# Kernel optimization log

Hardware: AMD Instinct MI355X
Metric: run time of the kernel (lower is better)

## Reference

```python
import jax, jax.numpy as jnp
import numpy as np

D = 1024
H = 16
HD = D // H
FF = 4 * D
EPS = 1e-5


def _layernorm(x, scale, shift):
    # Faithful to the torch module: unbiased std (ddof=1), eps added to std.
    mean = jnp.mean(x, axis=-1, keepdims=True)
    var = jnp.sum((x - mean) ** 2, axis=-1, keepdims=True) / (x.shape[-1] - 1)
    std = jnp.sqrt(var)
    return shift + scale * (x - mean) / (std + EPS)


def _gelu(x):
    c = jnp.sqrt(jnp.asarray(2.0 / jnp.pi, dtype=x.dtype))
    return 0.5 * x * (1.0 + jnp.tanh(c * (x + 0.044715 * x ** 3)))


def setup_inputs() -> dict:
    key = jax.random.key(0)
    ks = jax.random.split(key, 8)
    B, S = 2, 2048
    inv = 1.0 / np.sqrt(D)
    x = jax.random.normal(ks[0], (B, S, D), dtype=jnp.float32)
    scale1 = jnp.ones((D,), jnp.float32)
    shift1 = jnp.zeros((D,), jnp.float32)
    Wqkv = jax.random.normal(ks[1], (3 * D, D), jnp.float32) * inv  # torch layout [out,in]
    Wo_w = jax.random.normal(ks[2], (D, D), jnp.float32) * inv
    Wo_b = jnp.zeros((D,), jnp.float32)
    scale2 = jnp.ones((D,), jnp.float32)
    shift2 = jnp.zeros((D,), jnp.float32)
    W1 = jax.random.normal(ks[3], (FF, D), jnp.float32) * inv
    b1 = jnp.zeros((FF,), jnp.float32)
    W2 = jax.random.normal(ks[4], (D, FF), jnp.float32) * (1.0 / np.sqrt(FF))
    b2 = jnp.zeros((D,), jnp.float32)
    return {"x": x, "scale1": scale1, "shift1": shift1, "Wqkv": Wqkv,
            "Wo_w": Wo_w, "Wo_b": Wo_b, "scale2": scale2, "shift2": shift2,
            "W1": W1, "b1": b1, "W2": W2, "b2": b2}


def reference(x, scale1, shift1, Wqkv, Wo_w, Wo_b, scale2, shift2, W1, b1, W2, b2):
    B, S, _ = x.shape
    # --- pre-norm attention ---
    h = _layernorm(x, scale1, shift1)
    qkv = jnp.einsum('bsd,ed->bse', h, Wqkv)  # [B,S,3D]
    q, k, v = jnp.split(qkv, 3, axis=-1)
    q = q.reshape(B, S, H, HD).transpose(0, 2, 1, 3)  # [B,H,S,HD]
    k = k.reshape(B, S, H, HD).transpose(0, 2, 1, 3)
    v = v.reshape(B, S, H, HD).transpose(0, 2, 1, 3)
    scores = jnp.einsum('bhqd,bhkd->bhqk', q, k) / jnp.sqrt(jnp.asarray(HD, x.dtype))
    causal = jnp.triu(jnp.ones((S, S), dtype=bool), k=1)
    scores = jnp.where(causal, -jnp.inf, scores)
    weights = jax.nn.softmax(scores, axis=-1)
    attn = jnp.einsum('bhqk,bhkd->bhqd', weights, v)
    attn = attn.transpose(0, 2, 1, 3).reshape(B, S, D)
    attn = jnp.einsum('bsd,ed->bse', attn, Wo_w) + Wo_b
    x = x + attn
    # --- pre-norm MLP ---
    h2 = _layernorm(x, scale2, shift2)
    m = _gelu(jnp.einsum('bsd,fd->bsf', h2, W1) + b1)
    m = jnp.einsum('bsf,df->bsd', m, W2) + b2
    return x + m
```

## Files before the change

### kernel.cpp

```cpp
#include <hip/hip_runtime.h>
#include <cstdint>
#include <cstddef>

typedef __bf16 bf16;
typedef __bf16 v8bf __attribute__((ext_vector_type(8)));
typedef __bf16 v4bf __attribute__((ext_vector_type(4)));
typedef float  v4f  __attribute__((ext_vector_type(4)));

#define D_MODEL 1024
#define FF_DIM  4096
#define SEQ     2048
#define NTOK    4096
#define NH      16
#define HDIM    64

#define GLOAD_LDS16(g, l) \
    __builtin_amdgcn_global_load_lds((const __attribute__((address_space(1))) void*)(g), \
                                     (__attribute__((address_space(3))) void*)(l), 16, 0, 0)

#define QSCALE 0.18033688011112042f
#define SHIFT2 -28.853900817779268f

#define BARRIER()    asm volatile("s_barrier" ::: "memory")
#define WAIT_VM8()   asm volatile("s_waitcnt vmcnt(8)" ::: "memory")
#define WAIT_VM0()   asm volatile("s_waitcnt vmcnt(0)" ::: "memory")
#define WAIT_LGKM0() asm volatile("s_waitcnt lgkmcnt(0)" ::: "memory")

__global__ __launch_bounds__(256) void prep_kernel(
    const float* __restrict__ Wqkv, const float* __restrict__ Wo,
    const float* __restrict__ W1, const float* __restrict__ W2,
    bf16* __restrict__ Wqkv_b, bf16* __restrict__ Wo_b,
    bf16* __restrict__ W1_b, bf16* __restrict__ W2_b) {
    int u = blockIdx.x * 256 + threadIdx.x;
    const float* src; bf16* dst; int idx;
    if (u < 786432)       { src = Wqkv; dst = Wqkv_b; idx = u * 4; }
    else if (u < 1048576) { src = Wo;   dst = Wo_b;   idx = (u - 786432) * 4; }
    else if (u < 2097152) { src = W1;   dst = W1_b;   idx = (u - 1048576) * 4; }
    else                  { src = W2;   dst = W2_b;   idx = (u - 2097152) * 4; }
    float4 v = *(const float4*)(src + idx);
    dst[idx + 0] = (bf16)v.x;
    dst[idx + 1] = (bf16)v.y;
    dst[idx + 2] = (bf16)v.z;
    dst[idx + 3] = (bf16)v.w;
}

__global__ __launch_bounds__(256) void layernorm_kernel(
    const float* __restrict__ x, const float* __restrict__ scale,
    const float* __restrict__ shift, bf16* __restrict__ out) {
    int row = blockIdx.x;
    int t = threadIdx.x;
    const float* xr = x + (size_t)row * D_MODEL;
    float4 v = *(const float4*)(xr + t * 4);
    float s  = v.x + v.y + v.z + v.w;
    float sq = v.x * v.x + v.y * v.y + v.z * v.z + v.w * v.w;
    #pragma unroll
    for (int o = 1; o < 64; o <<= 1) {
        s  += __shfl_xor(s, o);
        sq += __shfl_xor(sq, o);
    }
    __shared__ float ws[8];
    int wv = t >> 6;
    if ((t & 63) == 0) { ws[wv * 2] = s; ws[wv * 2 + 1] = sq; }
    __syncthreads();
    s  = ws[0] + ws[2] + ws[4] + ws[6];
    sq = ws[1] + ws[3] + ws[5] + ws[7];
    float mean = s * (1.0f / D_MODEL);
    float var  = (sq - (float)D_MODEL * mean * mean) * (1.0f / (D_MODEL - 1));
    var = fmaxf(var, 0.0f);
    float inv = 1.0f / (sqrtf(var) + 1e-5f);
    #pragma unroll
    for (int j = 0; j < 4; ++j) {
        int c = t * 4 + j;
        float xv = (&v.x)[j];
        out[(size_t)row * D_MODEL + c] = (bf16)(shift[c] + scale[c] * (xv - mean) * inv);
    }
}

__global__ __launch_bounds__(256) void transpose_v(
    const bf16* __restrict__ vb, bf16* __restrict__ vt) {
    int bh = blockIdx.x >> 5;
    int ts = blockIdx.x & 31;
    int t = threadIdx.x;
    __shared__ bf16 T[64][72];
    const bf16* src = vb + ((size_t)bh * SEQ + ts * 64) * HDIM;
    #pragma unroll
    for (int half = 0; half < 2; ++half) {
        int s = (t >> 3) + half * 32;
        int d0 = (t & 7) * 8;
        v8bf vv = *(const v8bf*)(src + (size_t)s * HDIM + d0);
        #pragma unroll
        for (int j = 0; j < 8; ++j) T[d0 + j][s] = vv[j];
    }
    __syncthreads();
    bf16* dst = vt + (size_t)bh * HDIM * SEQ + ts * 64;
    int d = t >> 2;
    #pragma unroll
    for (int cc = 0; cc < 2; ++cc) {
        int c = (t & 3) + cc * 4;
        v8bf o = *(const v8bf*)(&T[d][c * 8]);
        *(v8bf*)(dst + (size_t)d * SEQ + c * 8) = o;
    }
}

template <int EPI>
__global__ __launch_bounds__(256) void gemm_nt(
    const bf16* __restrict__ A, const bf16* __restrict__ Bw,
    const float* __restrict__ bias, const float* __restrict__ resid,
    float* __restrict__ outf, bf16* __restrict__ ob0,
    bf16* __restrict__ ob1, bf16* __restrict__ ob2,
    int M, int N, int K, int klen) {
    __shared__ __align__(16) bf16 As[128 * 64];
    __shared__ __align__(16) bf16 Bs[128 * 64];
    int gx = gridDim.x;
    int lin = blockIdx.y * gx + blockIdx.x;
    int grpsz = 16 * gx;
    int group = lin / grpsz;
    int rem = lin - group * grpsz;
    int m_t = group * 16 + (rem & 15);
    int n_t = rem >> 4;
    int m0 = m_t * 128, n0 = n_t * 128;
    int kstart = blockIdx.z * klen;
    int t = threadIdx.x;
    int lane = t & 63, wave = t >> 6;
    int wm = wave >> 1, wn = wave & 1;
    int quad = lane >> 4, l16 = lane & 15;

    int srow8 = lane >> 3;
    int schunk = (lane & 7) ^ srow8;
    const bf16* agp = A  + (size_t)(m0 + wave * 8 + srow8) * K + kstart + schunk * 8;
    const bf16* bgp = Bw + (size_t)(n0 + wave * 8 + srow8) * K + kstart + schunk * 8;
    size_t row32 = (size_t)32 * K;

    v4f acc[4][4];
    #pragma unroll
    for (int i = 0; i < 4; ++i)
        #pragma unroll
        for (int j = 0; j < 4; ++j)
            acc[i][j] = (v4f){0.f, 0.f, 0.f, 0.f};

    int rsw = l16 & 7;
    for (int kk = 0; kk < klen; kk += 64) {
        __syncthreads();
        #pragma unroll
        for (int ii = 0; ii < 4; ++ii) {
            GLOAD_LDS16(agp + ii * row32 + kk, &As[ii * 2048 + wave * 512]);
            GLOAD_LDS16(bgp + ii * row32 + kk, &Bs[ii * 2048 + wave * 512]);
        }
        __syncthreads();
        #pragma unroll
        for (int h = 0; h < 2; ++h) {
            v8bf af[4], bfr[4];
            #pragma unroll
            for (int i = 0; i < 4; ++i)
                af[i] = *(const v8bf*)(&As[(wm * 64 + i * 16 + l16) * 64 + (((h * 4 + quad) ^ rsw)) * 8]);
            #pragma unroll
            for (int j = 0; j < 4; ++j)
                bfr[j] = *(const v8bf*)(&Bs[(wn * 64 + j * 16 + l16) * 64 + (((h * 4 + quad) ^ rsw)) * 8]);
            #pragma unroll
            for (int i = 0; i < 4; ++i)
                #pragma unroll
                for (int j = 0; j < 4; ++j)
                    acc[i][j] = __builtin_amdgcn_mfma_f32_16x16x32_bf16(af[i], bfr[j], acc[i][j], 0, 0, 0);
        }
    }

    #pragma unroll
    for (int i = 0; i < 4; ++i) {
        #pragma unroll
        for (int j = 0; j < 4; ++j) {
            #pragma unroll
            for (int r = 0; r < 4; ++r) {
                float v = acc[i][j][r];
                int row = m0 + wm * 64 + i * 16 + quad * 4 + r;
                int col = n0 + wn * 64 + j * 16 + l16;
                if (EPI == 1) {
                    size_t o = (size_t)row * N + col;
                    outf[o] = resid[o] + v + bias[col];
                }
            }
        }
    }
}

template <int EPI>
__global__ __launch_bounds__(512, 2) void gemm2_nt(
    const bf16* __restrict__ A, const bf16* __restrict__ Bw,
    const float* __restrict__ bias, bf16* __restrict__ ob0,
    bf16* __restrict__ ob1, bf16* __restrict__ ob2,
    int M, int N, int K, int klen) {
    __shared__ __align__(16) bf16 smA[2][256 * 64];
    __shared__ __align__(16) bf16 smB[2][256 * 64];

    int gx = gridDim.x, gy = gridDim.y;
    int nwg = gx * gy;
    int lin = blockIdx.y * gx + blockIdx.x;
    int q8 = nwg >> 3;
    int swz = (lin & 7) * q8 + (lin >> 3);
    int m_t = swz % gy;
    int n_t = swz / gy;
    int m0 = m_t * 256, n0 = n_t * 256;
    int kstart = blockIdx.z * klen;
    int t = threadIdx.x;
    int lane = t & 63, wave = t >> 6;
    int wm = wave >> 2, wn = wave & 3;
    int quad = lane >> 4, l16 = lane & 15;

    int srow8 = lane >> 3;
    int schunk = (lane & 7) ^ srow8;
    const bf16* aA = A  + (size_t)(m0 + wave * 8 + srow8) * K + kstart + schunk * 8;
    const bf16* bB = Bw + (size_t)(n0 + wave * 8 + srow8) * K + kstart + schunk * 8;
    size_t row64 = (size_t)64 * K;
    int NT = klen >> 6;

    v4f acc[8][4];
    #pragma unroll
    for (int i = 0; i < 8; ++i)
        #pragma unroll
        for (int j = 0; j < 4; ++j)
            acc[i][j] = (v4f){0.f, 0.f, 0.f, 0.f};

    auto stage = [&](int c, int kt) {
        size_t ko = (size_t)kt * 64;
        const bf16* ag = aA + ko;
        const bf16* bg = bB + ko;
        #pragma unroll
        for (int q = 0; q < 4; ++q) {
            GLOAD_LDS16(ag + q * row64, &smA[c][q * 4096 + wave * 512]);
            GLOAD_LDS16(bg + q * row64, &smB[c][q * 4096 + wave * 512]);
        }
    };

    stage(0, 0);
    if (NT > 1) { stage(1, 1); WAIT_VM8(); } else { WAIT_VM0(); }
    BARRIER();

    int rx = l16 & 7;
    int ch0 = (quad ^ rx) * 8;
    int ch1 = ch0 ^ 32;
    int arow = (wm * 128 + l16) * 64;
    int brow = (wn * 64 + l16) * 64;

    for (int kt = 0; kt < NT; ++kt) {
        int c = kt & 1;
        const bf16* Ab = &smA[c][arow];
        const bf16* Bb = &smB[c][brow];
        v8bf a[4][2], b[4][2];
        #pragma unroll
        for (int i = 0; i < 4; ++i) {
            a[i][0] = *(const v8bf*)(Ab + i * 1024 + ch0);
            a[i][1] = *(const v8bf*)(Ab + i * 1024 + ch1);
        }
        #pragma unroll
        for (int j = 0; j < 4; ++j) {
            b[j][0] = *(const v8bf*)(Bb + j * 1024 + ch0);
            b[j][1] = *(const v8bf*)(Bb + j * 1024 + ch1);
        }
        __builtin_amdgcn_s_setprio(1);
        #pragma unroll
        for (int i = 0; i < 4; ++i)
            #pragma unroll
            for (int j = 0; j < 2; ++j) {
                acc[i][j] = __builtin_amdgcn_mfma_f32_16x16x32_bf16(a[i][0], b[j][0], acc[i][j], 0, 0, 0);
                acc[i][j] = __builtin_amdgcn_mfma_f32_16x16x32_bf16(a[i][1], b[j][1], acc[i][j], 0, 0, 0);
            }
        __builtin_amdgcn_s_setprio(0);
        __builtin_amdgcn_s_setprio(1);
        #pragma unroll
        for (int i = 0; i < 4; ++i)
            #pragma unroll
            for (int j = 2; j < 4; ++j) {
                acc[i][j] = __builtin_amdgcn_mfma_f32_16x16x32_bf16(a[i][0], b[j][0], acc[i][j], 0, 0, 0);
                acc[i][j] = __builtin_amdgcn_mfma_f32_16x16x32_bf16(a[i][1], b[j][1], acc[i][j], 0, 0, 0);
            }
        __builtin_amdgcn_s_setprio(0);
        #pragma unroll
        for (int i = 0; i < 4; ++i) {
            a[i][0] = *(const v8bf*)(Ab + 4096 + i * 1024 + ch0);
            a[i][1] = *(const v8bf*)(Ab + 4096 + i * 1024 + ch1);
        }
        __builtin_amdgcn_s_setprio(1);
        #pragma unroll
        for (int i = 0; i < 4; ++i)
            #pragma unroll
            for (int j = 0; j < 2; ++j) {
                acc[i + 4][j] = __builtin_amdgcn_mfma_f32_16x16x32_bf16(a[i][0], b[j][0], acc[i + 4][j], 0, 0, 0);
                acc[i + 4][j] = __builtin_amdgcn_mfma_f32_16x16x32_bf16(a[i][1], b[j][1], acc[i + 4][j], 0, 0, 0);
            }
        __builtin_amdgcn_s_setprio(0);
        WAIT_LGKM0();
        BARRIER();
        if (kt + 2 < NT) stage(c, kt + 2);
        __builtin_amdgcn_s_setprio(1);
        #pragma unroll
        for (int i = 0; i < 4; ++i)
            #pragma unroll
            for (int j = 2; j < 4; ++j) {
                acc[i + 4][j] = __builtin_amdgcn_mfma_f32_16x16x32_bf16(a[i][0], b[j][0], acc[i + 4][j], 0, 0, 0);
                acc[i + 4][j] = __builtin_amdgcn_mfma_f32_16x16x32_bf16(a[i][1], b[j][1], acc[i + 4][j], 0, 0, 0);
            }
        __builtin_amdgcn_s_setprio(0);
        if (kt + 1 < NT) {
            if (kt + 2 < NT) WAIT_VM8();
            else             WAIT_VM0();
            BARRIER();
        }
    }

    #pragma unroll
    for (int i = 0; i < 8; ++i) {
        #pragma unroll
        for (int j = 0; j < 4; ++j) {
            #pragma unroll
            for (int r = 0; r < 4; ++r) {
                float v = acc[i][j][r];
                int row = m0 + wm * 128 + i * 16 + quad * 4 + r;
                int col = n0 + wn * 64 + j * 16 + l16;
                if (EPI == 0) {
                    int which = col >> 10, rr = col & 1023;
                    int h = rr >> 6, d = rr & 63;
                    int bb = row >> 11, sI = row & 2047;
                    size_t dst = (((size_t)(bb * NH + h)) * SEQ + sI) * HDIM + d;
                    if (which == 0)      ob0[dst] = (bf16)(v * QSCALE);
                    else if (which == 1) ob1[dst] = (bf16)v;
                    else                 ob2[dst] = (bf16)v;
                } else if (EPI == 2) {
                    float u = v + bias[col];
                    float y = 1.5957691216057308f * (u + 0.044715f * u * u * u);
                    float g = u * __builtin_amdgcn_rcpf(1.0f + __expf(-y));
                    ob0[(size_t)row * N + col] = (bf16)g;
                } else {
                    ob0[(size_t)blockIdx.z * M * N + (size_t)row * N + col] = (bf16)v;
                }
            }
        }
    }
}

__global__ __launch_bounds__(256) void combine_w2(
    const bf16* __restrict__ part, const float* __restrict__ x1,
    const float* __restrict__ b2, float* __restrict__ out) {
    int i = (blockIdx.x * 256 + threadIdx.x) * 4;
    int col = i & (D_MODEL - 1);
    float4 xv = *(const float4*)(x1 + i);
    float4 bv = *(const float4*)(b2 + col);
    float4 r;
    r.x = xv.x + bv.x; r.y = xv.y + bv.y; r.z = xv.z + bv.z; r.w = xv.w + bv.w;
    #pragma unroll
    for (int z = 0; z < 4; ++z) {
        v4bf p = *(const v4bf*)(part + (size_t)z * NTOK * D_MODEL + i);
        r.x += (float)p[0]; r.y += (float)p[1]; r.z += (float)p[2]; r.w += (float)p[3];
    }
    *(float4*)(out + i) = r;
}

__device__ __forceinline__ void attn_process_tile(
    int kv, int qwb, int quad, int l16,
    const bf16* Ks, const bf16* Vs, bf16* Pw, const v8bf& ones,
    const v8bf& qf0, const v8bf& qf1, v4f (&o)[4], v4f& o5) {
    #pragma unroll
    for (int hh = 0; hh < 2; ++hh) {
        int kb32 = kv + hh * 32;
        if (kb32 > qwb + 15) break;
        #pragma unroll
        for (int j2 = 0; j2 < 2; ++j2) {
            int j = hh * 2 + j2;
            int kb16 = kb32 + j2 * 16;
            union { bf16 h[4]; uint2 u; } pk;
            if (kb16 > qwb + 15) {
                pk.u = (uint2){0u, 0u};
            } else {
                int key = j * 16 + l16;
                v8bf ka = *(const v8bf*)(&Ks[(key * 8 + (quad ^ (key & 7))) * 8]);
                v8bf kc = *(const v8bf*)(&Ks[(key * 8 + ((quad + 4) ^ (key & 7))) * 8]);
                v4f s = (v4f){SHIFT2, SHIFT2, SHIFT2, SHIFT2};
                s = __builtin_amdgcn_mfma_f32_16x16x32_bf16(ka, qf0, s, 0, 0, 0);
                s = __builtin_amdgcn_mfma_f32_16x16x32_bf16(kc, qf1, s, 0, 0, 0);
                bool dm = (kb16 + 15 > qwb);
                int keyb = kb16 + quad * 4;
                #pragma unroll
                for (int r = 0; r < 4; ++r) {
                    float pv = __builtin_amdgcn_exp2f(s[r]);
                    if (dm) pv = (keyb + r <= qwb + l16) ? pv : 0.f;
                    pk.h[r] = (bf16)pv;
                }
            }
            *(uint2*)(&Pw[l16 * 72 + j * 16 + quad * 4]) = pk.u;
        }
        v8bf pf = *(const v8bf*)(&Pw[l16 * 72 + hh * 32 + quad * 8]);
        o5 = __builtin_amdgcn_mfma_f32_16x16x32_bf16(pf, ones, o5, 0, 0, 0);
        #pragma unroll
        for (int dc = 0; dc < 4; ++dc) {
            int dim = dc * 16 + l16;
            v8bf vv = *(const v8bf*)(&Vs[(dim * 8 + ((quad + 4 * hh) ^ (dim & 7))) * 8]);
            o[dc] = __builtin_amdgcn_mfma_f32_16x16x32_bf16(pf, vv, o[dc], 0, 0, 0);
        }
    }
}

__global__ __launch_bounds__(512, 4) void attn_kernel(
    const bf16* __restrict__ qb, const bf16* __restrict__ kb,
    const bf16* __restrict__ vt, bf16* __restrict__ ob) {
    int bh = blockIdx.x & 31;
    int pr = blockIdx.x >> 5;
    int qtA = pr, qtB = 31 - pr;

    int t = threadIdx.x;
    int wave = t >> 6, lane = t & 63;
    int g = wave >> 2, wv = wave & 3;
    int quad = lane >> 4, l16 = lane & 15;
    int qwbA = qtA * 64 + wv * 16;
    int qwbB = qtB * 64 + wv * 16;

    const bf16* Qh  = qb + (size_t)bh * SEQ * HDIM;
    const bf16* Kh  = kb + (size_t)bh * SEQ * HDIM;
    const bf16* Vth = vt + (size_t)bh * HDIM * SEQ;

    __shared__ __align__(16) char smem_raw[51200];
    bf16* Ks  = (bf16*)smem_raw;
    bf16* Vs  = (bf16*)(smem_raw + 16384);
    bf16* Pw  = (bf16*)(smem_raw + 32768) + wave * 1152;
    float* scr = (float*)smem_raw;

    int key = t >> 3;
    int cch = (t & 7) ^ (key & 7);
    const bf16* Ksrc = Kh + (size_t)key * HDIM + cch * 8;
    const bf16* Vsrc = Vth + (size_t)key * SEQ + cch * 8;
    bf16* kdst0 = Ks + wave * 512;
    bf16* kdst1 = Ks + 4096 + wave * 512;
    bf16* vdst0 = Vs + wave * 512;
    bf16* vdst1 = Vs + 4096 + wave * 512;

    v8bf qfA0 = *(const v8bf*)(Qh + (size_t)(qwbA + l16) * HDIM + quad * 8);
    v8bf qfA1 = *(const v8bf*)(Qh + (size_t)(qwbA + l16) * HDIM + 32 + quad * 8);
    v8bf qfB0 = *(const v8bf*)(Qh + (size_t)(qwbB + l16) * HDIM + quad * 8);
    v8bf qfB1 = *(const v8bf*)(Qh + (size_t)(qwbB + l16) * HDIM + 32 + quad * 8);

    v8bf ones;
    #pragma unroll
    for (int j = 0; j < 8; ++j) ones[j] = (bf16)1.0f;

    v4f oA[4], oB[4];
    #pragma unroll
    for (int dc = 0; dc < 4; ++dc) {
        oA[dc] = (v4f){0.f, 0.f, 0.f, 0.f};
        oB[dc] = (v4f){0.f, 0.f, 0.f, 0.f};
    }
    v4f o5A = (v4f){0.f, 0.f, 0.f, 0.f};
    v4f o5B = (v4f){0.f, 0.f, 0.f, 0.f};

    int nt = qtB + 1;
    int nit = (nt + 1) >> 1;
    for (int it = 0; it < nit; ++it) {
        int t0 = 2 * it;
        int t1 = t0 + 1;
        __syncthreads();
        GLOAD_LDS16(Ksrc + (size_t)(t0 * 64) * HDIM, kdst0);
        GLOAD_LDS16(Vsrc + t0 * 64, vdst0);
        if (t1 < nt) {
            GLOAD_LDS16(Ksrc + (size_t)(t1 * 64) * HDIM, kdst1);
            GLOAD_LDS16(Vsrc + t1 * 64, vdst1);
        }
        __syncthreads();
        int ti = t0 + g;
        if (ti < nt) {
            int kv = ti * 64;
            const bf16* Kst = Ks + g * 4096;
            const bf16* Vst = Vs + g * 4096;
            if (ti <= qtA)
                attn_process_tile(kv, qwbA, quad, l16, Kst, Vst, Pw, ones,
                                  qfA0, qfA1, oA, o5A);
            attn_process_tile(kv, qwbB, quad, l16, Kst, Vst, Pw, ones,
                              qfB0, qfB1, oB, o5B);
        }
    }

    __syncthreads();
    int sbase = wv * 2560 + lane;
    if (g == 1) {
        #pragma unroll
        for (int dc = 0; dc < 4; ++dc)
            #pragma unroll
            for (int r = 0; r < 4; ++r) {
                scr[sbase + (dc * 4 + r) * 64]        = oA[dc][r];
                scr[sbase + (16 + dc * 4 + r) * 64]   = oB[dc][r];
            }
        #pragma unroll
        for (int r = 0; r < 4; ++r) {
            scr[sbase + (32 + r) * 64] = o5A[r];
            scr[sbase + (36 + r) * 64] = o5B[r];
        }
    }
    __syncthreads();
    if (g == 0) {
        #pragma unroll
        for (int dc = 0; dc < 4; ++dc)
            #pragma unroll
            for (int r = 0; r < 4; ++r) {
                oA[dc][r] += scr[sbase + (dc * 4 + r) * 64];
                oB[dc][r] += scr[sbase + (16 + dc * 4 + r) * 64];
            }
        #pragma unroll
        for (int r = 0; r < 4; ++r) {
            o5A[r] += scr[sbase + (32 + r) * 64];
            o5B[r] += scr[sbase + (36 + r) * 64];
        }
        int b = bh >> 4, h = bh & 15;
        #pragma unroll
        for (int r = 0; r < 4; ++r) {
            float invA = 1.0f / o5A[r];
            float invB = 1.0f / o5B[r];
            int sA = qwbA + quad * 4 + r;
            int sB = qwbB + quad * 4 + r;
            #pragma unroll
            for (int dc = 0; dc < 4; ++dc) {
                int d = dc * 16 + l16;
                ob[((size_t)(b * SEQ + sA)) * D_MODEL + h * HDIM + d] = (bf16)(oA[dc][r] * invA);
                ob[((size_t)(b * SEQ + sB)) * D_MODEL + h * HDIM + d] = (bf16)(oB[dc][r] * invB);
            }
        }
    }
}

extern "C" void kernel_launch(void* const* d_in, const int* in_sizes, int n_in,
                              void* d_out, int out_size, void* d_ws, size_t ws_size,
                              hipStream_t stream) {
    const float* x      = (const float*)d_in[0];
    const float* scale1 = (const float*)d_in[1];
    const float* shift1 = (const float*)d_in[2];
    const float* Wqkv   = (const float*)d_in[3];
    const float* Wo_w   = (const float*)d_in[4];
    const float* Wo_b   = (const float*)d_in[5];
    const float* scale2 = (const float*)d_in[6];
    const float* shift2 = (const float*)d_in[7];
    const float* W1     = (const float*)d_in[8];
    const float* b1     = (const float*)d_in[9];
    const float* W2     = (const float*)d_in[10];
    const float* b2     = (const float*)d_in[11];
    float* out = (float*)d_out;

    char* ws = (char*)d_ws;
    size_t off = 0;
    auto alloc = [&](size_t bytes) -> char* {
        char* p = ws + off;
        off += (bytes + 255) & ~(size_t)255;
        return p;
    };
    bf16* Wqkv_b = (bf16*)alloc((size_t)3 * D_MODEL * D_MODEL * 2);
    bf16* Wo_bf  = (bf16*)alloc((size_t)D_MODEL * D_MODEL * 2);
    bf16* W1_b   = (bf16*)alloc((size_t)FF_DIM * D_MODEL * 2);
    bf16* W2_b   = (bf16*)alloc((size_t)D_MODEL * FF_DIM * 2);
    bf16* bufA   = (bf16*)alloc((size_t)NTOK * D_MODEL * 2);
    bf16* qb     = (bf16*)alloc((size_t)NTOK * D_MODEL * 2);
    bf16* kb     = (bf16*)alloc((size_t)NTOK * D_MODEL * 2);
    bf16* vb     = (bf16*)alloc((size_t)NTOK * D_MODEL * 2);
    bf16* vtb    = (bf16*)alloc((size_t)NTOK * D_MODEL * 2);
    float* x1    = (float*)alloc((size_t)NTOK * D_MODEL * 4);
    bf16* mbuf   = (bf16*)alloc((size_t)NTOK * FF_DIM * 2);
    bf16* w2part = bufA;
    (void)ws_size; (void)n_in; (void)in_sizes; (void)out_size;

    prep_kernel<<<12288, 256, 0, stream>>>(Wqkv, Wo_w, W1, W2,
                                           Wqkv_b, Wo_bf, W1_b, W2_b);

    layernorm_kernel<<<NTOK, 256, 0, stream>>>(x, scale1, shift1, bufA);

    gemm2_nt<0><<<dim3(3072 / 256, NTOK / 256), 512, 0, stream>>>(
        bufA, Wqkv_b, nullptr, qb, kb, vb, NTOK, 3072, D_MODEL, D_MODEL);

    transpose_v<<<1024, 256, 0, stream>>>(vb, vtb);

    attn_kernel<<<512, 512, 0, stream>>>(qb, kb, vtb, bufA);

    gemm_nt<1><<<dim3(D_MODEL / 128, NTOK / 128), 256, 0, stream>>>(
        bufA, Wo_bf, Wo_b, x, x1, nullptr, nullptr, nullptr, NTOK, D_MODEL, D_MODEL, D_MODEL);

    layernorm_kernel<<<NTOK, 256, 0, stream>>>(x1, scale2, shift2, qb);

    gemm2_nt<2><<<dim3(FF_DIM / 256, NTOK / 256), 512, 0, stream>>>(
        qb, W1_b, b1, mbuf, nullptr, nullptr, NTOK, FF_DIM, D_MODEL, D_MODEL);

    gemm2_nt<6><<<dim3(D_MODEL / 256, NTOK / 256, 4), 512, 0, stream>>>(
        mbuf, W2_b, nullptr, w2part, nullptr, nullptr, NTOK, D_MODEL, FF_DIM, FF_DIM / 4);

    combine_w2<<<NTOK * D_MODEL / 1024, 256, 0, stream>>>(w2part, x1, b2, out);
}
```

Baseline: 314.6 us.

## Replace two-stage BK=64 GEMM pipeline with four-stage BK=32 LDS ring

Restructures the 256x256 gemm2_nt main loop. The old version double-buffered 64-wide K tiles; the new one uses a 4-slot ring of 32-wide K tiles, prefetching three tiles ahead, with one barrier per iteration and vmcnt waits tuned to the number of outstanding stages. The goal is to hide global-load latency better and simplify the interleaved MFMA/LDS schedule. The cost is twice as many barriers per K and fewer MFMAs between them. The prologue also assumes at least three K tiles.

```diff
diff --git a/kernel.cpp b/kernel.cpp
--- a/kernel.cpp
+++ b/kernel.cpp
@@ -23,6 +23,7 @@
 
 #define BARRIER()    asm volatile("s_barrier" ::: "memory")
 #define WAIT_VM8()   asm volatile("s_waitcnt vmcnt(8)" ::: "memory")
+#define WAIT_VM4()   asm volatile("s_waitcnt vmcnt(4)" ::: "memory")
 #define WAIT_VM0()   asm volatile("s_waitcnt vmcnt(0)" ::: "memory")
 #define WAIT_LGKM0() asm volatile("s_waitcnt lgkmcnt(0)" ::: "memory")
 
@@ -188,8 +189,8 @@
     const float* __restrict__ bias, bf16* __restrict__ ob0,
     bf16* __restrict__ ob1, bf16* __restrict__ ob2,
     int M, int N, int K, int klen) {
-    __shared__ __align__(16) bf16 smA[2][256 * 64];
-    __shared__ __align__(16) bf16 smB[2][256 * 64];
+    __shared__ __align__(16) bf16 smA[4][256 * 32];
+    __shared__ __align__(16) bf16 smB[4][256 * 32];
 
     int gx = gridDim.x, gy = gridDim.y;
     int nwg = gx * gy;
@@ -205,12 +206,12 @@
     int wm = wave >> 2, wn = wave & 3;
     int quad = lane >> 4, l16 = lane & 15;
 
-    int srow8 = lane >> 3;
-    int schunk = (lane & 7) ^ srow8;
-    const bf16* aA = A  + (size_t)(m0 + wave * 8 + srow8) * K + kstart + schunk * 8;
-    const bf16* bB = Bw + (size_t)(n0 + wave * 8 + srow8) * K + kstart + schunk * 8;
-    size_t row64 = (size_t)64 * K;
-    int NT = klen >> 6;
+    int srow = t >> 2;
+    int sch  = (t & 3) ^ (srow & 3);
+    const bf16* aA = A  + (size_t)(m0 + srow) * K + kstart + sch * 8;
+    const bf16* bB = Bw + (size_t)(n0 + srow) * K + kstart + sch * 8;
+    size_t row128 = (size_t)128 * K;
+    int NT = klen >> 5;
 
     v4f acc[8][4];
     #pragma unroll
@@ -219,89 +220,48 @@
         for (int j = 0; j < 4; ++j)
             acc[i][j] = (v4f){0.f, 0.f, 0.f, 0.f};
 
-    auto stage = [&](int c, int kt) {
-        size_t ko = (size_t)kt * 64;
-        const bf16* ag = aA + ko;
-        const bf16* bg = bB + ko;
-        #pragma unroll
-        for (int q = 0; q < 4; ++q) {
-            GLOAD_LDS16(ag + q * row64, &smA[c][q * 4096 + wave * 512]);
-            GLOAD_LDS16(bg + q * row64, &smB[c][q * 4096 + wave * 512]);
-        }
+    auto stage = [&](int s, int kt) {
+        size_t ko = (size_t)kt * 32;
+        GLOAD_LDS16(aA + ko,          &smA[s][wave * 512]);
+        GLOAD_LDS16(aA + row128 + ko, &smA[s][4096 + wave * 512]);
+        GLOAD_LDS16(bB + ko,          &smB[s][wave * 512]);
+        GLOAD_LDS16(bB + row128 + ko, &smB[s][4096 + wave * 512]);
     };
 
     stage(0, 0);
-    if (NT > 1) { stage(1, 1); WAIT_VM8(); } else { WAIT_VM0(); }
+    stage(1, 1);
+    stage(2, 2);
+    WAIT_VM8();
     BARRIER();
 
-    int rx = l16 & 7;
-    int ch0 = (quad ^ rx) * 8;
-    int ch1 = ch0 ^ 32;
-    int arow = (wm * 128 + l16) * 64;
-    int brow = (wn * 64 + l16) * 64;
+    int sl = (quad ^ (l16 & 3)) * 8;
+    int arow = (wm * 128 + l16) * 32;
+    int brow = (wn * 64 + l16) * 32;
 
     for (int kt = 0; kt < NT; ++kt) {
-        int c = kt & 1;
-        const bf16* Ab = &smA[c][arow];
-        const bf16* Bb = &smB[c][brow];
-        v8bf a[4][2], b[4][2];
-        #pragma unroll
-        for (int i = 0; i < 4; ++i) {
-            a[i][0] = *(const v8bf*)(Ab + i * 1024 + ch0);
-            a[i][1] = *(const v8bf*)(Ab + i * 1024 + ch1);
-        }
-        #pragma unroll
-        for (int j = 0; j < 4; ++j) {
-            b[j][0] = *(const v8bf*)(Bb + j * 1024 + ch0);
-            b[j][1] = *(const v8bf*)(Bb + j * 1024 + ch1);
-        }
+        int s = kt & 3;
+        if (kt + 3 < NT) stage((kt + 3) & 3, kt + 3);
+        const bf16* Ab = &smA[s][arow + sl];
+        const bf16* Bb = &smB[s][brow + sl];
+        v8bf a[8], bfr[4];
+        #pragma unroll
+        for (int i = 0; i < 8; ++i)
+            a[i] = *(const v8bf*)(Ab + i * 512);
+        #pragma unroll
+        for (int j = 0; j < 4; ++j)
+            bfr[j] = *(const v8bf*)(Bb + j * 512);
         __builtin_amdgcn_s_setprio(1);
         #pragma unroll
-        for (int i = 0; i < 4; ++i)
-            #pragma unroll
-            for (int j = 0; j < 2; ++j) {
-                acc[i][j] = __builtin_amdgcn_mfma_f32_16x16x32_bf16(a[i][0], b[j][0], acc[i][j], 0, 0, 0);
-                acc[i][j] = __builtin_amdgcn_mfma_f32_16x16x32_bf16(a[i][1], b[j][1], acc[i][j], 0, 0, 0);
-            }
-        __builtin_amdgcn_s_setprio(0);
-        __builtin_amdgcn_s_setprio(1);
-        #pragma unroll
-        for (int i = 0; i < 4; ++i)
-            #pragma unroll
-            for (int j = 2; j < 4; ++j) {
-                acc[i][j] = __builtin_amdgcn_mfma_f32_16x16x32_bf16(a[i][0], b[j][0], acc[i][j], 0, 0, 0);
-                acc[i][j] = __builtin_amdgcn_mfma_f32_16x16x32_bf16(a[i][1], b[j][1], acc[i][j], 0, 0, 0);
-            }
-        __builtin_amdgcn_s_setprio(0);
-        #pragma unroll
-        for (int i = 0; i < 4; ++i) {
-            a[i][0] = *(const v8bf*)(Ab + 4096 + i * 1024 + ch0);
-            a[i][1] = *(const v8bf*)(Ab + 4096 + i * 1024 + ch1);
-        }
-        __builtin_amdgcn_s_setprio(1);
-        #pragma unroll
-        for (int i = 0; i < 4; ++i)
-            #pragma unroll
-            for (int j = 0; j < 2; ++j) {
-                acc[i + 4][j] = __builtin_amdgcn_mfma_f32_16x16x32_bf16(a[i][0], b[j][0], acc[i + 4][j], 0, 0, 0);
-                acc[i + 4][j] = __builtin_amdgcn_mfma_f32_16x16x32_bf16(a[i][1], b[j][1], acc[i + 4][j], 0, 0, 0);
-            }
-        __builtin_amdgcn_s_setprio(0);
-        WAIT_LGKM0();
-        BARRIER();
-        if (kt + 2 < NT) stage(c, kt + 2);
-        __builtin_amdgcn_s_setprio(1);
-        #pragma unroll
-        for (int i = 0; i < 4; ++i)
-            #pragma unroll
-            for (int j = 2; j < 4; ++j) {
-                acc[i + 4][j] = __builtin_amdgcn_mfma_f32_16x16x32_bf16(a[i][0], b[j][0], acc[i + 4][j], 0, 0, 0);
-                acc[i + 4][j] = __builtin_amdgcn_mfma_f32_16x16x32_bf16(a[i][1], b[j][1], acc[i + 4][j], 0, 0, 0);
-            }
+        for (int i = 0; i < 8; ++i)
+            #pragma unroll
+            for (int j = 0; j < 4; ++j)
+                acc[i][j] = __builtin_amdgcn_mfma_f32_16x16x32_bf16(a[i], bfr[j], acc[i][j], 0, 0, 0);
         __builtin_amdgcn_s_setprio(0);
         if (kt + 1 < NT) {
-            if (kt + 2 < NT) WAIT_VM8();
-            else             WAIT_VM0();
+            WAIT_LGKM0();
+            if (kt + 4 <= NT)      WAIT_VM8();
+            else if (kt + 3 == NT) WAIT_VM4();
+            else                   WAIT_VM0();
             BARRIER();
         }
     }
```

New measurement: 349.4 us. 11.0% more time.

## Interleave GEMM prefetch slices with MFMA phases using extra barriers and sched fences

Applied to the files above, without the earlier changes.

Restructures the main GEMM k-loop so the next-tile global-to-LDS loads are split into slices and issued between the four MFMA phases, instead of all at once mid-loop. It also defers loading half of the B fragments, adds workgroup barriers around each phase so waves stay in lockstep, and puts scheduling fences so the compiler keeps the LDS reads separate from the MFMA blocks. The goal is to spread memory traffic across the compute and keep the matrix units busy. The cost is many more barriers per iteration, which may stall waves. The code also drops the guard for NT==1 in the prologue.

```diff
diff --git a/kernel.cpp b/kernel.cpp
--- a/kernel.cpp
+++ b/kernel.cpp
@@ -25,6 +25,7 @@
 #define WAIT_VM8()   asm volatile("s_waitcnt vmcnt(8)" ::: "memory")
 #define WAIT_VM0()   asm volatile("s_waitcnt vmcnt(0)" ::: "memory")
 #define WAIT_LGKM0() asm volatile("s_waitcnt lgkmcnt(0)" ::: "memory")
+#define SCHED_FENCE() __builtin_amdgcn_sched_barrier(0)
 
 __global__ __launch_bounds__(256) void prep_kernel(
     const float* __restrict__ Wqkv, const float* __restrict__ Wo,
@@ -219,89 +220,118 @@
         for (int j = 0; j < 4; ++j)
             acc[i][j] = (v4f){0.f, 0.f, 0.f, 0.f};
 
-    auto stage = [&](int c, int kt) {
-        size_t ko = (size_t)kt * 64;
-        const bf16* ag = aA + ko;
-        const bf16* bg = bB + ko;
-        #pragma unroll
-        for (int q = 0; q < 4; ++q) {
-            GLOAD_LDS16(ag + q * row64, &smA[c][q * 4096 + wave * 512]);
-            GLOAD_LDS16(bg + q * row64, &smB[c][q * 4096 + wave * 512]);
-        }
+    auto stageA = [&](int b, int q, int kt) {
+        GLOAD_LDS16(aA + (size_t)q * row64 + (size_t)kt * 64,
+                    &smA[b][q * 4096 + wave * 512]);
     };
-
-    stage(0, 0);
-    if (NT > 1) { stage(1, 1); WAIT_VM8(); } else { WAIT_VM0(); }
+    auto stageB = [&](int b, int q, int kt) {
+        GLOAD_LDS16(bB + (size_t)q * row64 + (size_t)kt * 64,
+                    &smB[b][q * 4096 + wave * 512]);
+    };
+
+    #pragma unroll
+    for (int q = 0; q < 4; ++q) { stageA(0, q, 0); stageB(0, q, 0); }
+    #pragma unroll
+    for (int q = 0; q < 4; ++q) { stageA(1, q, 1); stageB(1, q, 1); }
+    WAIT_VM8();
     BARRIER();
 
     int rx = l16 & 7;
     int ch0 = (quad ^ rx) * 8;
     int ch1 = ch0 ^ 32;
-    int arow = (wm * 128 + l16) * 64;
-    int brow = (wn * 64 + l16) * 64;
+    int aq_lo = (2 * wm) * 4096;
+    int aq_hi = aq_lo + 4096;
+    int bq    = wn * 4096;
 
     for (int kt = 0; kt < NT; ++kt) {
-        int c = kt & 1;
-        const bf16* Ab = &smA[c][arow];
-        const bf16* Bb = &smB[c][brow];
-        v8bf a[4][2], b[4][2];
+        int b = kt & 1;
+        bool pf = (kt + 2 < NT);
+        const bf16* Ab = &smA[b][0];
+        const bf16* Bb = &smB[b][0];
+        v8bf a[4][2], blo[2][2], bhi[2][2];
+
         #pragma unroll
         for (int i = 0; i < 4; ++i) {
-            a[i][0] = *(const v8bf*)(Ab + i * 1024 + ch0);
-            a[i][1] = *(const v8bf*)(Ab + i * 1024 + ch1);
-        }
-        #pragma unroll
-        for (int j = 0; j < 4; ++j) {
-            b[j][0] = *(const v8bf*)(Bb + j * 1024 + ch0);
-            b[j][1] = *(const v8bf*)(Bb + j * 1024 + ch1);
-        }
+            a[i][0] = *(const v8bf*)(Ab + aq_lo + (i * 16 + l16) * 64 + ch0);
+            a[i][1] = *(const v8bf*)(Ab + aq_lo + (i * 16 + l16) * 64 + ch1);
+        }
+        #pragma unroll
+        for (int j = 0; j < 2; ++j) {
+            blo[j][0] = *(const v8bf*)(Bb + bq + (j * 16 + l16) * 64 + ch0);
+            blo[j][1] = *(const v8bf*)(Bb + bq + (j * 16 + l16) * 64 + ch1);
+        }
+        BARRIER();
+        WAIT_LGKM0();
+        SCHED_FENCE();
         __builtin_amdgcn_s_setprio(1);
         #pragma unroll
         for (int i = 0; i < 4; ++i)
             #pragma unroll
             for (int j = 0; j < 2; ++j) {
-                acc[i][j] = __builtin_amdgcn_mfma_f32_16x16x32_bf16(a[i][0], b[j][0], acc[i][j], 0, 0, 0);
-                acc[i][j] = __builtin_amdgcn_mfma_f32_16x16x32_bf16(a[i][1], b[j][1], acc[i][j], 0, 0, 0);
+                acc[i][j] = __builtin_amdgcn_mfma_f32_16x16x32_bf16(a[i][0], blo[j][0], acc[i][j], 0, 0, 0);
+                acc[i][j] = __builtin_amdgcn_mfma_f32_16x16x32_bf16(a[i][1], blo[j][1], acc[i][j], 0, 0, 0);
             }
         __builtin_amdgcn_s_setprio(0);
+        BARRIER();
+
+        #pragma unroll
+        for (int j = 0; j < 2; ++j) {
+            bhi[j][0] = *(const v8bf*)(Bb + bq + ((j + 2) * 16 + l16) * 64 + ch0);
+            bhi[j][1] = *(const v8bf*)(Bb + bq + ((j + 2) * 16 + l16) * 64 + ch1);
+        }
+        if (pf) { stageA(b, 0, kt + 2); stageA(b, 2, kt + 2); }
+        BARRIER();
+        WAIT_LGKM0();
+        SCHED_FENCE();
         __builtin_amdgcn_s_setprio(1);
         #pragma unroll
         for (int i = 0; i < 4; ++i)
             #pragma unroll
-            for (int j = 2; j < 4; ++j) {
-                acc[i][j] = __builtin_amdgcn_mfma_f32_16x16x32_bf16(a[i][0], b[j][0], acc[i][j], 0, 0, 0);
-                acc[i][j] = __builtin_amdgcn_mfma_f32_16x16x32_bf16(a[i][1], b[j][1], acc[i][j], 0, 0, 0);
+            for (int j = 0; j < 2; ++j) {
+                acc[i][j + 2] = __builtin_amdgcn_mfma_f32_16x16x32_bf16(a[i][0], bhi[j][0], acc[i][j + 2], 0, 0, 0);
+                acc[i][j + 2] = __builtin_amdgcn_mfma_f32_16x16x32_bf16(a[i][1], bhi[j][1], acc[i][j + 2], 0, 0, 0);
             }
         __builtin_amdgcn_s_setprio(0);
+        BARRIER();
+
         #pragma unroll
         for (int i = 0; i < 4; ++i) {
-            a[i][0] = *(const v8bf*)(Ab + 4096 + i * 1024 + ch0);
-            a[i][1] = *(const v8bf*)(Ab + 4096 + i * 1024 + ch1);
-        }
+            a[i][0] = *(const v8bf*)(Ab + aq_hi + (i * 16 + l16) * 64 + ch0);
+            a[i][1] = *(const v8bf*)(Ab + aq_hi + (i * 16 + l16) * 64 + ch1);
+        }
+        if (pf) {
+            stageB(b, 0, kt + 2); stageB(b, 1, kt + 2);
+            stageB(b, 2, kt + 2); stageB(b, 3, kt + 2);
+        }
+        BARRIER();
+        WAIT_LGKM0();
+        SCHED_FENCE();
         __builtin_amdgcn_s_setprio(1);
         #pragma unroll
         for (int i = 0; i < 4; ++i)
             #pragma unroll
             for (int j = 0; j < 2; ++j) {
-                acc[i + 4][j] = __builtin_amdgcn_mfma_f32_16x16x32_bf16(a[i][0], b[j][0], acc[i + 4][j], 0, 0, 0);
-                acc[i + 4][j] = __builtin_amdgcn_mfma_f32_16x16x32_bf16(a[i][1], b[j][1], acc[i + 4][j], 0, 0, 0);
+                acc[i + 4][j] = __builtin_amdgcn_mfma_f32_16x16x32_bf16(a[i][0], blo[j][0], acc[i + 4][j], 0, 0, 0);
+                acc[i + 4][j] = __builtin_amdgcn_mfma_f32_16x16x32_bf16(a[i][1], blo[j][1], acc[i + 4][j], 0, 0, 0);
             }
         __builtin_amdgcn_s_setprio(0);
-        WAIT_LGKM0();
         BARRIER();
-        if (kt + 2 < NT) stage(c, kt + 2);
+
+        if (pf) { stageA(b, 1, kt + 2); stageA(b, 3, kt + 2); }
+        BARRIER();
+        SCHED_FENCE();
         __builtin_amdgcn_s_setprio(1);
         #pragma unroll
         for (int i = 0; i < 4; ++i)
             #pragma unroll
-            for (int j = 2; j < 4; ++j) {
-                acc[i + 4][j] = __builtin_amdgcn_mfma_f32_16x16x32_bf16(a[i][0], b[j][0], acc[i + 4][j], 0, 0, 0);
-                acc[i + 4][j] = __builtin_amdgcn_mfma_f32_16x16x32_bf16(a[i][1], b[j][1], acc[i + 4][j], 0, 0, 0);
+            for (int j = 0; j < 2; ++j) {
+                acc[i + 4][j + 2] = __builtin_amdgcn_mfma_f32_16x16x32_bf16(a[i][0], bhi[j][0], acc[i + 4][j + 2], 0, 0, 0);
+                acc[i + 4][j + 2] = __builtin_amdgcn_mfma_f32_16x16x32_bf16(a[i][1], bhi[j][1], acc[i + 4][j + 2], 0, 0, 0);
             }
         __builtin_amdgcn_s_setprio(0);
         if (kt + 1 < NT) {
-            if (kt + 2 < NT) WAIT_VM8();
-            else             WAIT_VM0();
+            if (pf) WAIT_VM8();
+            else    WAIT_VM0();
             BARRIER();
         }
     }
```

Result: slower. 325.2 us (+3.3%).

## Prefetch next K/V tile pair into registers during attention compute

Applied to the files above, without the earlier changes.

Replaces the direct global-to-LDS loads with register-staged loads. The next pair of K/V tiles is fetched into registers before the current tiles are processed, then written to LDS after a barrier. The goal is to hide global memory latency behind the MFMA work instead of stalling on the load at the start of each iteration. In exchange it uses more registers, adds an explicit LDS write step, and keeps two barriers per iteration.

```diff
diff --git a/kernel.cpp b/kernel.cpp
--- a/kernel.cpp
+++ b/kernel.cpp
@@ -425,10 +425,10 @@
     int cch = (t & 7) ^ (key & 7);
     const bf16* Ksrc = Kh + (size_t)key * HDIM + cch * 8;
     const bf16* Vsrc = Vth + (size_t)key * SEQ + cch * 8;
-    bf16* kdst0 = Ks + wave * 512;
-    bf16* kdst1 = Ks + 4096 + wave * 512;
-    bf16* vdst0 = Vs + wave * 512;
-    bf16* vdst1 = Vs + 4096 + wave * 512;
+    bf16* kdst0 = Ks + t * 8;
+    bf16* kdst1 = Ks + 4096 + t * 8;
+    bf16* vdst0 = Vs + t * 8;
+    bf16* vdst1 = Vs + 4096 + t * 8;
 
     v8bf qfA0 = *(const v8bf*)(Qh + (size_t)(qwbA + l16) * HDIM + quad * 8);
     v8bf qfA1 = *(const v8bf*)(Qh + (size_t)(qwbA + l16) * HDIM + 32 + quad * 8);
@@ -449,18 +449,33 @@
     v4f o5B = (v4f){0.f, 0.f, 0.f, 0.f};
 
     int nt = qtB + 1;
+
+    uint4 rk0, rk1, rv0, rv1;
+    auto loadpair = [&](int t0) {
+        rk0 = *(const uint4*)(Ksrc + (size_t)(t0 * 64) * HDIM);
+        rv0 = *(const uint4*)(Vsrc + t0 * 64);
+        if (t0 + 1 < nt) {
+            rk1 = *(const uint4*)(Ksrc + (size_t)((t0 + 1) * 64) * HDIM);
+            rv1 = *(const uint4*)(Vsrc + (t0 + 1) * 64);
+        }
+    };
+    auto writepair = [&](int t0) {
+        *(uint4*)kdst0 = rk0;
+        *(uint4*)vdst0 = rv0;
+        if (t0 + 1 < nt) {
+            *(uint4*)kdst1 = rk1;
+            *(uint4*)vdst1 = rv1;
+        }
+    };
+
+    loadpair(0);
+    writepair(0);
+    __syncthreads();
+
     int nit = (nt + 1) >> 1;
     for (int it = 0; it < nit; ++it) {
         int t0 = 2 * it;
-        int t1 = t0 + 1;
-        __syncthreads();
-        GLOAD_LDS16(Ksrc + (size_t)(t0 * 64) * HDIM, kdst0);
-        GLOAD_LDS16(Vsrc + t0 * 64, vdst0);
-        if (t1 < nt) {
-            GLOAD_LDS16(Ksrc + (size_t)(t1 * 64) * HDIM, kdst1);
-            GLOAD_LDS16(Vsrc + t1 * 64, vdst1);
-        }
-        __syncthreads();
+        if (t0 + 2 < nt) loadpair(t0 + 2);
         int ti = t0 + g;
         if (ti < nt) {
             int kv = ti * 64;
@@ -472,6 +487,9 @@
             attn_process_tile(kv, qwbB, quad, l16, Kst, Vst, Pw, ones,
                               qfB0, qfB1, oB, o5B);
         }
+        __syncthreads();
+        if (t0 + 2 < nt) writepair(t0 + 2);
+        __syncthreads();
     }
 
     __syncthreads();
```

Measured after the change: 321.2 us. +2.1%, slower.
